# Kernel tuning notes

Measured on AMD Instinct MI355X. Metric: run time of the kernel, lower is better.

The kernel has to match this reference:

```python
import jax, jax.numpy as jnp
import numpy as np

# Module hyperparameters (see init_kwargs)
P1, P2 = 32, 32      # num_patches_h, num_patches_w (256/8)
H1, W2 = 8, 8        # patch_size
CH = 3               # input channels
CI, SI = 768, 4      # num_cores, rfs_per_capsule (capsule_size=256, rf_size=64)
KOUT, LOUT = 256, 4  # output_cores, slots per output core
PROBA = 0.1          # connection_proba


def setup_inputs() -> dict:
    key = jax.random.key(0)
    kx, kc = jax.random.split(key)
    x = jax.random.normal(kx, (128, 256, 256, 3), dtype=jnp.float32)
    # fast_scrramble: fixed random-sparse binary connectivity tensor
    # [source_core, source_slot, dest_core, dest_slot]
    C = jax.random.bernoulli(kc, PROBA, (CI, SI, KOUT, LOUT)).astype(jnp.float32)
    return {"x": x, "C": C}


def reference(x, C):
    b = x.shape[0]
    # 'b (p1 h1) (p2 w2) c -> b p1 p2 h1 w2 c'
    x = x.reshape(b, P1, H1, P2, W2, CH).transpose(0, 1, 3, 2, 4, 5)
    # 'b p1 p2 h1 w2 c -> b h1 w2 (p1 p2 c)'
    x = x.transpose(0, 3, 4, 1, 2, 5).reshape(b, H1, W2, P1 * P2 * CH)
    # 'b h1 w2 (ci si) -> b ci si h1 w2'
    x = x.reshape(b, H1, W2, CI, SI).transpose(0, 3, 4, 1, 2)
    # Literal einsum from the source: no shared labels between operands,
    # so this is sum_{c,s} x (per b,h,w) times sum_{i,j} C (per k,l).
    return jnp.einsum('bcshw,ijkl->bklhw', x, C)
```

## Files before the change

### kernel.cpp

```cpp
#include <hip/hip_runtime.h>


#define PSX_ELEMS (128 * 8 * 64)
#define PSC_ELEMS (96 * 1024)

__global__ __launch_bounds__(256) void reduce_C_part(const float* __restrict__ C,
                                                     float4* __restrict__ psC) {
    const int p = blockIdx.x;
    const int t = threadIdx.x;
    const float4* row = (const float4*)(C + (size_t)p * 32 * 1024) + t;
    float4 a = {0.f, 0.f, 0.f, 0.f};
#pragma unroll
    for (int r = 0; r < 32; ++r) {
        float4 v = row[(size_t)r * 256];
        a.x += v.x; a.y += v.y; a.z += v.z; a.w += v.w;
    }
    psC[p * 256 + t] = a;
}

__global__ __launch_bounds__(384) void reduce_x_part(const float* __restrict__ x,
                                                     const float* __restrict__ psC,
                                                     float* __restrict__ psx,
                                                     float* __restrict__ sC) {
    const int b  = blockIdx.y;
    const int bx = blockIdx.x;
    const int t  = threadIdx.x;
    const float4* base4 = (const float4*)(x + ((size_t)b * 256 + bx * 32) * 768);

    float4 acc[4];
#pragma unroll
    for (int mm = 0; mm < 4; ++mm) acc[mm] = (float4){0.f, 0.f, 0.f, 0.f};

#pragma unroll
    for (int jj = 0; jj < 4; ++jj)
#pragma unroll
        for (int mm = 0; mm < 4; ++mm) {
            float4 v = base4[(size_t)(mm + 4 * jj) * 384 + t];
            acc[mm].x += v.x; acc[mm].y += v.y; acc[mm].z += v.z; acc[mm].w += v.w;
        }

    __shared__ float4 lds4[8][193];
    const int r  = t / 192;
    const int c4 = t % 192;
#pragma unroll
    for (int mm = 0; mm < 4; ++mm) lds4[2 * mm + r][c4] = acc[mm];
    __syncthreads();

    if (t < 64) {
        const int h = t >> 3, w = t & 7;
        const float* L = (const float*)&lds4[h][0];
        float s = 0.f;
#pragma unroll
        for (int g = 0; g < 32; ++g)
            s += L[3 * w + 24 * g] + L[3 * w + 1 + 24 * g] + L[3 * w + 2 + 24 * g];
        psx[(size_t)b * 512 + bx * 64 + t] = s;
    }

    if (b == 0 && t < 128) {
        const int col = bx * 128 + t;
        float s = 0.f;
#pragma unroll
        for (int p = 0; p < 96; ++p) s += psC[p * 1024 + col];
        sC[col] = s;
    }
}

__global__ __launch_bounds__(256) void expand_kernel(const float* __restrict__ psx,
                                                     const float* __restrict__ sC,
                                                     float4* __restrict__ out) {
    const int b  = blockIdx.y;
    const int bx = blockIdx.x;
    const int t  = threadIdx.x;

    __shared__ float4 sxl4[16];
    __shared__ float  sCl[64];

    if (t < 64) {
        float s = 0.f;
#pragma unroll
        for (int g = 0; g < 8; ++g) s += psx[(size_t)b * 512 + g * 64 + t];
        ((float*)sxl4)[t] = s;
    } else if (t < 128) {
        sCl[t - 64] = sC[bx * 64 + (t - 64)];
    }
    __syncthreads();

    const float4 v = sxl4[t & 15];
    float4* ob = out + (size_t)b * 16384 + bx * 1024 + t;
#pragma unroll
    for (int u = 0; u < 4; ++u) {
        const float s = sCl[(t >> 4) + 16 * u];
        float4 rr; rr.x = v.x * s; rr.y = v.y * s; rr.z = v.z * s; rr.w = v.w * s;
        ob[256 * u] = rr;
    }
}

extern "C" void kernel_launch(void* const* d_in, const int* in_sizes, int n_in,
                              void* d_out, int out_size, void* d_ws, size_t ws_size,
                              hipStream_t stream) {
    const float* x = (const float*)d_in[0];
    const float* C = (const float*)d_in[1];
    float* out = (float*)d_out;

    float* psx = (float*)d_ws;
    float* psC = psx + PSX_ELEMS;
    float* sC  = psC + PSC_ELEMS;

    reduce_C_part<<<dim3(96), 256, 0, stream>>>(C, (float4*)psC);
    reduce_x_part<<<dim3(8, 128), 384, 0, stream>>>(x, psC, psx, sC);
    expand_kernel<<<dim3(16, 128), 256, 0, stream>>>(psx, sC, (float4*)out);
}
```

Baseline: 189.2 us.

## Split x reduction into row-sum pass and separate finalize kernel

Replaces the fused x-reduction kernel, which reduced 16 rows per block and then did an LDS channel/patch reduction, with a simple streaming kernel. That kernel sums 32 rows per (batch, h) into a rowsum buffer, and a new small finalize kernel then computes the per-(h,w) sums and the C column sums. The aim is simpler, fully coalesced streaming of the large x tensor with fewer registers and no LDS. The cost is an extra kernel launch and a 3 MB intermediate round trip through global memory.

```diff
diff --git a/kernel.cpp b/kernel.cpp
--- a/kernel.cpp
+++ b/kernel.cpp
@@ -1,14 +1,14 @@
 #include <hip/hip_runtime.h>
 
 
-#define PSX_ELEMS (128 * 8 * 64)
-#define PSC_ELEMS (96 * 1024)
+#define ROWSUM_ELEMS (128 * 8 * 768)
+#define PSC_ELEMS    (96 * 1024)
 
 __global__ __launch_bounds__(256) void reduce_C_part(const float* __restrict__ C,
                                                      float4* __restrict__ psC) {
     const int p = blockIdx.x;
     const int t = threadIdx.x;
-    const float4* row = (const float4*)(C + (size_t)p * 32 * 1024) + t;
+    const float4* row = (const float4*)C + (size_t)p * 32 * 256 + t;
     float4 a = {0.f, 0.f, 0.f, 0.f};
 #pragma unroll
     for (int r = 0; r < 32; ++r) {
@@ -18,46 +18,38 @@
     psC[p * 256 + t] = a;
 }
 
-__global__ __launch_bounds__(384) void reduce_x_part(const float* __restrict__ x,
-                                                     const float* __restrict__ psC,
-                                                     float* __restrict__ psx,
-                                                     float* __restrict__ sC) {
-    const int b  = blockIdx.y;
-    const int bx = blockIdx.x;
-    const int t  = threadIdx.x;
-    const float4* base4 = (const float4*)(x + ((size_t)b * 256 + bx * 32) * 768);
+__global__ __launch_bounds__(192) void reduce_rows(const float* __restrict__ x,
+                                                   float4* __restrict__ rowsum) {
+    const int blk = blockIdx.x;
+    const int b = blk >> 3, h = blk & 7;
+    const int t = threadIdx.x;
+    const float4* xb = (const float4*)x + (size_t)b * 49152 + (size_t)h * 192 + t;
+    float4 a = {0.f, 0.f, 0.f, 0.f};
+#pragma unroll
+    for (int j = 0; j < 32; ++j) {
+        float4 v = xb[(size_t)j * 1536];
+        a.x += v.x; a.y += v.y; a.z += v.z; a.w += v.w;
+    }
+    rowsum[(size_t)blk * 192 + t] = a;
+}
 
-    float4 acc[4];
+__global__ __launch_bounds__(128) void finalize(const float* __restrict__ rowsum,
+                                                const float* __restrict__ psC,
+                                                float* __restrict__ sx,
+                                                float* __restrict__ sC) {
+    const int blk = blockIdx.x, t = threadIdx.x;
+    if (blk < 128) {
+        if (t < 64) {
+            const int h = t >> 3, w = t & 7;
+            const float* r = rowsum + (size_t)blk * 6144 + h * 768 + 3 * w;
+            float s = 0.f;
 #pragma unroll
-    for (int mm = 0; mm < 4; ++mm) acc[mm] = (float4){0.f, 0.f, 0.f, 0.f};
-
-#pragma unroll
-    for (int jj = 0; jj < 4; ++jj)
-#pragma unroll
-        for (int mm = 0; mm < 4; ++mm) {
-            float4 v = base4[(size_t)(mm + 4 * jj) * 384 + t];
-            acc[mm].x += v.x; acc[mm].y += v.y; acc[mm].z += v.z; acc[mm].w += v.w;
+            for (int g = 0; g < 32; ++g)
+                s += r[24 * g] + r[24 * g + 1] + r[24 * g + 2];
+            sx[blk * 64 + t] = s;
         }
-
-    __shared__ float4 lds4[8][193];
-    const int r  = t / 192;
-    const int c4 = t % 192;
-#pragma unroll
-    for (int mm = 0; mm < 4; ++mm) lds4[2 * mm + r][c4] = acc[mm];
-    __syncthreads();
-
-    if (t < 64) {
-        const int h = t >> 3, w = t & 7;
-        const float* L = (const float*)&lds4[h][0];
-        float s = 0.f;
-#pragma unroll
-        for (int g = 0; g < 32; ++g)
-            s += L[3 * w + 24 * g] + L[3 * w + 1 + 24 * g] + L[3 * w + 2 + 24 * g];
-        psx[(size_t)b * 512 + bx * 64 + t] = s;
-    }
-
-    if (b == 0 && t < 128) {
-        const int col = bx * 128 + t;
+    } else {
+        const int col = (blk - 128) * 128 + t;
         float s = 0.f;
 #pragma unroll
         for (int p = 0; p < 96; ++p) s += psC[p * 1024 + col];
@@ -65,27 +57,17 @@
     }
 }
 
-__global__ __launch_bounds__(256) void expand_kernel(const float* __restrict__ psx,
+__global__ __launch_bounds__(256) void expand_kernel(const float* __restrict__ sx,
                                                      const float* __restrict__ sC,
                                                      float4* __restrict__ out) {
-    const int b  = blockIdx.y;
-    const int bx = blockIdx.x;
-    const int t  = threadIdx.x;
-
-    __shared__ float4 sxl4[16];
-    __shared__ float  sCl[64];
-
-    if (t < 64) {
-        float s = 0.f;
-#pragma unroll
-        for (int g = 0; g < 8; ++g) s += psx[(size_t)b * 512 + g * 64 + t];
-        ((float*)sxl4)[t] = s;
-    } else if (t < 128) {
-        sCl[t - 64] = sC[bx * 64 + (t - 64)];
-    }
+    const int b = blockIdx.y, bx = blockIdx.x, t = threadIdx.x;
+    __shared__ float sxl[64];
+    __shared__ float sCl[64];
+    if (t < 64)       sxl[t]      = sx[b * 64 + t];
+    else if (t < 128) sCl[t - 64] = sC[bx * 64 + (t - 64)];
     __syncthreads();
 
-    const float4 v = sxl4[t & 15];
+    const float4 v = ((const float4*)sxl)[t & 15];
     float4* ob = out + (size_t)b * 16384 + bx * 1024 + t;
 #pragma unroll
     for (int u = 0; u < 4; ++u) {
@@ -102,11 +84,13 @@
     const float* C = (const float*)d_in[1];
     float* out = (float*)d_out;
 
-    float* psx = (float*)d_ws;
-    float* psC = psx + PSX_ELEMS;
-    float* sC  = psC + PSC_ELEMS;
+    float* rowsum = (float*)d_ws;
+    float* psC    = rowsum + ROWSUM_ELEMS;
+    float* sC     = psC + PSC_ELEMS;
+    float* sx     = sC + 1024;
 
-    reduce_C_part<<<dim3(96), 256, 0, stream>>>(C, (float4*)psC);
-    reduce_x_part<<<dim3(8, 128), 384, 0, stream>>>(x, psC, psx, sC);
-    expand_kernel<<<dim3(16, 128), 256, 0, stream>>>(psx, sC, (float4*)out);
+    reduce_C_part<<<dim3(96),      256, 0, stream>>>(C, (float4*)psC);
+    reduce_rows  <<<dim3(1024),    192, 0, stream>>>(x, (float4*)rowsum);
+    finalize     <<<dim3(136),     128, 0, stream>>>(rowsum, psC, sx, sC);
+    expand_kernel<<<dim3(16, 128), 256, 0, stream>>>(sx, sC, (float4*)out);
 }
```

Measured after the change: 192.4 us. About the same (+1.7%).
